# Kernel optimization log

Hardware: AMD Instinct MI355X
Metric: run time of the kernel (lower is better)

## Reference

```python
import jax, jax.numpy as jnp
import numpy as np

D = 1024
H = 16
DK = D // H
FF = int(8 / 3 * D)  # 2730
EPS = 1e-6


def setup_inputs() -> dict:
    key = jax.random.key(0)
    ks = jax.random.split(key, 8)
    s = lambda n: 1.0 / np.sqrt(n)
    return {
        "x": jax.random.normal(ks[0], (2, 2048, D), dtype=jnp.float32),
        "w_qkv": jax.random.normal(ks[1], (3 * D, D), dtype=jnp.float32) * s(D),
        "w_o": jax.random.normal(ks[2], (D, D), dtype=jnp.float32) * s(D),
        "n1_w": jnp.ones((D,), dtype=jnp.float32),
        "n2_w": jnp.ones((D,), dtype=jnp.float32),
        "w1": jax.random.normal(ks[3], (FF, D), dtype=jnp.float32) * s(D),
        "w2": jax.random.normal(ks[4], (D, FF), dtype=jnp.float32) * s(FF),
        "w3": jax.random.normal(ks[5], (FF, D), dtype=jnp.float32) * s(D),
    }


def _rmsnorm(x, w):
    return x * jax.lax.rsqrt(jnp.mean(x * x, axis=-1, keepdims=True) + EPS) * w


def _attn(x, w_qkv, w_o):
    B, L, _ = x.shape
    qkv = x @ w_qkv.T                       # [B,L,3D]
    qkv = qkv.reshape(B, L, 3, H, DK)
    q, k, v = qkv[:, :, 0], qkv[:, :, 1], qkv[:, :, 2]   # [B,L,H,DK]
    scores = jnp.einsum("blhd,bmhd->bhlm", q, k) / np.sqrt(DK).astype(np.float32)
    attn = jax.nn.softmax(scores, axis=-1)               # [B,H,L,L]
    out = jnp.einsum("bhlm,bmhd->blhd", attn, v).reshape(B, L, D)
    return out @ w_o.T


def _swiglu(x, w1, w2, w3):
    return (jax.nn.silu(x @ w1.T) * (x @ w3.T)) @ w2.T


def reference(x, w_qkv, w_o, n1_w, n2_w, w1, w2, w3):
    x = x + _attn(_rmsnorm(x, n1_w), w_qkv, w_o)
    return x + _swiglu(_rmsnorm(x, n2_w), w1, w2, w3)
```

## Files before the change

kernel.cpp:

```cpp
#include <hip/hip_runtime.h>
#include <stdint.h>


#define LSEQ   2048
#define DMODEL 1024
#define NHEAD  16
#define NTOK   4096
#define FFR    2730
#define FFP    2816
#define FF2    5632

typedef short  short8  __attribute__((ext_vector_type(8)));
typedef float  floatx4 __attribute__((ext_vector_type(4)));

__device__ __forceinline__ uint16_t f2bf(float f) {
  uint32_t u = __builtin_bit_cast(uint32_t, f);
  u += 0x7FFFu + ((u >> 16) & 1u);
  return (uint16_t)(u >> 16);
}
__device__ __forceinline__ float bf2f(uint16_t s) {
  uint32_t u = ((uint32_t)s) << 16;
  return __builtin_bit_cast(float, u);
}
__device__ __forceinline__ void gl2lds16(const void* g, void* l) {
  __builtin_amdgcn_global_load_lds(
      (const __attribute__((address_space(1))) unsigned int*)g,
      (__attribute__((address_space(3))) unsigned int*)l, 16, 0, 0);
}

__global__ __launch_bounds__(256) void cvt_all_k(const float* __restrict__ wqkv,
                                                 const float* __restrict__ wo,
                                                 const float* __restrict__ w1,
                                                 const float* __restrict__ w3,
                                                 uint16_t* __restrict__ dst) {
  int g = blockIdx.x;
  int c = threadIdx.x * 4;
  const float* src = nullptr;
  if (g < 3072)       src = wqkv + (size_t)g * 1024;
  else if (g < 4096)  src = wo + (size_t)(g - 3072) * 1024;
  else {
    int r = g - 4096;
    int u = r >> 6, wi = r & 63;
    int srow = u * 32 + (wi & 31);
    if (srow < FFR) src = ((wi < 32) ? w1 : w3) + (size_t)srow * 1024;
  }
  float4 v = src ? *(const float4*)(src + c) : float4{0, 0, 0, 0};
  uint64_t pack =  (uint64_t)f2bf(v.x)        | ((uint64_t)f2bf(v.y) << 16)
                | ((uint64_t)f2bf(v.z) << 32) | ((uint64_t)f2bf(v.w) << 48);
  *(uint64_t*)(dst + (size_t)g * 1024 + c) = pack;
}

__global__ void cvt_pad_k(const float* __restrict__ src, uint16_t* __restrict__ dst,
                          int rows, int cols, int cols_p, long total) {
  long idx = (long)blockIdx.x * 256 + threadIdx.x;
  if (idx >= total) return;
  int r = (int)(idx / cols_p);
  int c = (int)(idx % cols_p);
  float v = (r < rows && c < cols) ? src[(size_t)r * cols + c] : 0.0f;
  dst[idx] = f2bf(v);
}

__global__ __launch_bounds__(256) void rmsnorm_k(const float* __restrict__ x,
                                                 const float* __restrict__ wgt,
                                                 uint16_t* __restrict__ out) {
  const int row = blockIdx.x;
  const int c = threadIdx.x * 4;
  const float* xr = x + (size_t)row * DMODEL;
  float4 v = *(const float4*)(xr + c);
  float ss = v.x * v.x + v.y * v.y + v.z * v.z + v.w * v.w;
#pragma unroll
  for (int off = 32; off >= 1; off >>= 1) ss += __shfl_down(ss, off, 64);
  __shared__ float red[4];
  if ((threadIdx.x & 63) == 0) red[threadIdx.x >> 6] = ss;
  __syncthreads();
  float tot = red[0] + red[1] + red[2] + red[3];
  float scale = rsqrtf(tot * (1.0f / DMODEL) + 1e-6f);
  float4 wv = *(const float4*)(wgt + c);
  uint64_t pack =  (uint64_t)f2bf(v.x * scale * wv.x)
                | ((uint64_t)f2bf(v.y * scale * wv.y) << 16)
                | ((uint64_t)f2bf(v.z * scale * wv.z) << 32)
                | ((uint64_t)f2bf(v.w * scale * wv.w) << 48);
  *(uint64_t*)(out + (size_t)row * DMODEL + c) = pack;
}

template <int MODE, int TM, int TN>
__global__ __launch_bounds__(256) void gemm_bt(const uint16_t* __restrict__ A,
                                               const uint16_t* __restrict__ B,
                                               uint16_t* __restrict__ Cb,
                                               float* __restrict__ Cf,
                                               const float* __restrict__ Res,
                                               int M, int N, int K) {
  constexpr int FI = TM / 32, FJ = TN / 32;
  constexpr int NIT = (TM + TN) / 64;
  __shared__ uint16_t As[TM * 32];
  __shared__ uint16_t Bs[TN * 32];
  const int tid = threadIdx.x;
  const int w = tid >> 6, lane = tid & 63;
  const int grp = lane >> 4, l16 = lane & 15;
  const int m0 = blockIdx.y * TM, n0 = blockIdx.x * TN;
  const int rw = (w >> 1) * (TM / 2), cw = (w & 1) * (TN / 2);

  floatx4 acc[FI][FJ] = {};

  const uint16_t* gp[NIT];
  uint16_t* lp[NIT];
#pragma unroll
  for (int i = 0; i < NIT; i++) {
    int c = i * 256 + tid;
    if (c < TM * 4) {
      gp[i] = A + (size_t)(m0 + (c >> 2)) * K + (c & 3) * 8;
      lp[i] = As + c * 8;
    } else {
      int c2 = c - TM * 4;
      gp[i] = B + (size_t)(n0 + (c2 >> 2)) * K + (c2 & 3) * 8;
      lp[i] = Bs + c2 * 8;
    }
  }

  for (int k0 = 0; k0 < K; k0 += 32) {
#pragma unroll
    for (int i = 0; i < NIT; i++) gl2lds16(gp[i] + k0, lp[i]);
    __syncthreads();
    short8 af[FI], bfr[FJ];
#pragma unroll
    for (int i = 0; i < FI; i++)
      af[i] = *(const short8*)(As + (rw + i * 16 + l16) * 32 + grp * 8);
#pragma unroll
    for (int j = 0; j < FJ; j++)
      bfr[j] = *(const short8*)(Bs + (cw + j * 16 + l16) * 32 + grp * 8);
#pragma unroll
    for (int i = 0; i < FI; i++)
#pragma unroll
      for (int j = 0; j < FJ; j++)
        acc[i][j] = __builtin_amdgcn_mfma_f32_16x16x32_bf16(af[i], bfr[j], acc[i][j], 0, 0, 0);
    __syncthreads();
  }

  if constexpr (MODE == 2) {
    const int half = N >> 1;
#pragma unroll
    for (int i = 0; i < FI; i++) {
      const int mrow = m0 + rw + i * 16 + grp * 4;
#pragma unroll
      for (int j = 0; j < 2; j++) {
        const int gcol = (n0 >> 1) + (cw >> 1) + j * 16 + l16;
#pragma unroll
        for (int r = 0; r < 4; r++) {
          float a = acc[i][j][r];
          float bv = acc[i][j + 2][r];
          float ex = __builtin_amdgcn_exp2f(-a * 1.4426950408889634f);
          float s = a * __builtin_amdgcn_rcpf(1.0f + ex);
          Cb[(size_t)(mrow + r) * half + gcol] = f2bf(s * bv);
        }
      }
    }
  } else {
#pragma unroll
    for (int i = 0; i < FI; i++) {
#pragma unroll
      for (int j = 0; j < FJ; j++) {
        const int mrow = m0 + rw + i * 16 + grp * 4;
        const int ncol = n0 + cw + j * 16 + l16;
#pragma unroll
        for (int r = 0; r < 4; r++) {
          size_t idx = (size_t)(mrow + r) * N + ncol;
          float v = acc[i][j][r];
          if (MODE == 0) Cb[idx] = f2bf(v);
          else           Cf[idx] = v + Res[idx];
        }
      }
    }
  }
}

__global__ __launch_bounds__(256) void attn_flash(const uint16_t* __restrict__ qkv,
                                                  uint16_t* __restrict__ outp) {
  const int tid = threadIdx.x;
  const int w = tid >> 6, lane = tid & 63;
  const int grp = lane >> 4, l16 = lane & 15;
  const int lin = blockIdx.x;
  const int xcd = lin & 7;
  const int slot = lin >> 3;
  const int pair = xcd * 4 + (slot >> 4);
  const int qc = slot & 15;
  const int h = pair & 15, b = pair >> 4;
  const int q0 = qc * 128;

  __shared__ uint16_t Qs[8192];
  __shared__ uint16_t Ks[2][4096];
  __shared__ uint16_t Vt[2][64 * 76];
  __shared__ uint16_t Ps[128 * 76];

  const size_t base = ((size_t)b * LSEQ) * 3072 + (size_t)h * 64;

#pragma unroll
  for (int i = 0; i < 4; i++) {
    int c = i * 256 + tid;
    int row = c >> 3, cc = (c & 7) ^ (row & 7);
    gl2lds16(qkv + base + (size_t)(q0 + row) * 3072 + cc * 8, Qs + c * 8);
  }
#pragma unroll
  for (int i = 0; i < 2; i++) {
    int c = i * 256 + tid;
    int row = c >> 3, cc = (c & 7) ^ (row & 7);
    gl2lds16(qkv + base + (size_t)row * 3072 + 1024 + cc * 8, Ks[0] + c * 8);
  }
#pragma unroll
  for (int i = 0; i < 2; i++) {
    int c = i * 256 + tid;
    int tt = c & 63, db = c >> 6;
    uint4 vv = *(const uint4*)(qkv + base + (size_t)tt * 3072 + 2048 + db * 8);
    uint32_t uu[4] = {vv.x, vv.y, vv.z, vv.w};
#pragma unroll
    for (int e = 0; e < 4; e++) {
      Vt[0][(db * 8 + e * 2 + 0) * 76 + tt] = (uint16_t)(uu[e] & 0xFFFFu);
      Vt[0][(db * 8 + e * 2 + 1) * 76 + tt] = (uint16_t)(uu[e] >> 16);
    }
  }
  __syncthreads();

  short8 aq[2][2];
#pragma unroll
  for (int fi = 0; fi < 2; fi++) {
    const int qrow = w * 32 + fi * 16 + l16;
#pragma unroll
    for (int kk = 0; kk < 2; kk++) {
      int cc = kk * 4 + grp;
      aq[fi][kk] = *(const short8*)(Qs + (qrow * 8 + (cc ^ (qrow & 7))) * 8);
    }
  }

  float lsum[2][4] = {};
  floatx4 o_acc[2][4] = {};
  const float C = 0.125f * 1.4426950408889634f;

  for (int kc = 0; kc < LSEQ / 64; kc++) {
    const int cur = kc & 1, nxt = cur ^ 1;
    const bool pre = (kc + 1 < LSEQ / 64);
    const int t1 = (kc + 1) * 64;
    uint4 vv[2];
    if (pre) {
#pragma unroll
      for (int i = 0; i < 2; i++) {
        int c = i * 256 + tid;
        int row = c >> 3, cc = (c & 7) ^ (row & 7);
        gl2lds16(qkv + base + (size_t)(t1 + row) * 3072 + 1024 + cc * 8, Ks[nxt] + c * 8);
      }
#pragma unroll
      for (int i = 0; i < 2; i++) {
        int c = i * 256 + tid;
        int tt = c & 63, db = c >> 6;
        vv[i] = *(const uint4*)(qkv + base + (size_t)(t1 + tt) * 3072 + 2048 + db * 8);
      }
    }

    floatx4 s_acc[2][4] = {};
#pragma unroll
    for (int j = 0; j < 4; j++) {
      const int krow = j * 16 + l16;
#pragma unroll
      for (int kk = 0; kk < 2; kk++) {
        int cc = kk * 4 + grp;
        short8 bk = *(const short8*)(Ks[cur] + (krow * 8 + (cc ^ (krow & 7))) * 8);
#pragma unroll
        for (int fi = 0; fi < 2; fi++)
          s_acc[fi][j] = __builtin_amdgcn_mfma_f32_16x16x32_bf16(aq[fi][kk], bk, s_acc[fi][j], 0, 0, 0);
      }
    }

#pragma unroll
    for (int fi = 0; fi < 2; fi++) {
      const int prow = w * 32 + fi * 16 + grp * 4;
#pragma unroll
      for (int j = 0; j < 4; j++)
#pragma unroll
        for (int r = 0; r < 4; r++) {
          float pv = __builtin_amdgcn_exp2f(s_acc[fi][j][r] * C);
          lsum[fi][r] += pv;
          Ps[(prow + r) * 76 + j * 16 + l16] = f2bf(pv);
        }
    }

#pragma unroll
    for (int kk = 0; kk < 2; kk++) {
      short8 ap0 = *(const short8*)(Ps + (w * 32 + l16) * 76 + kk * 32 + grp * 8);
      short8 ap1 = *(const short8*)(Ps + (w * 32 + 16 + l16) * 76 + kk * 32 + grp * 8);
#pragma unroll
      for (int jj = 0; jj < 4; jj++) {
        short8 bv = *(const short8*)(Vt[cur] + (jj * 16 + l16) * 76 + kk * 32 + grp * 8);
        o_acc[0][jj] = __builtin_amdgcn_mfma_f32_16x16x32_bf16(ap0, bv, o_acc[0][jj], 0, 0, 0);
        o_acc[1][jj] = __builtin_amdgcn_mfma_f32_16x16x32_bf16(ap1, bv, o_acc[1][jj], 0, 0, 0);
      }
    }

    if (pre) {
#pragma unroll
      for (int i = 0; i < 2; i++) {
        int c = i * 256 + tid;
        int tt = c & 63, db = c >> 6;
        uint32_t uu[4] = {vv[i].x, vv[i].y, vv[i].z, vv[i].w};
#pragma unroll
        for (int e = 0; e < 4; e++) {
          Vt[nxt][(db * 8 + e * 2 + 0) * 76 + tt] = (uint16_t)(uu[e] & 0xFFFFu);
          Vt[nxt][(db * 8 + e * 2 + 1) * 76 + tt] = (uint16_t)(uu[e] >> 16);
        }
      }
    }
    __syncthreads();
  }

#pragma unroll
  for (int off = 8; off >= 1; off >>= 1)
#pragma unroll
    for (int fi = 0; fi < 2; fi++)
#pragma unroll
      for (int r = 0; r < 4; r++) lsum[fi][r] += __shfl_xor(lsum[fi][r], off, 64);
#pragma unroll
  for (int fi = 0; fi < 2; fi++)
#pragma unroll
    for (int jj = 0; jj < 4; jj++)
#pragma unroll
      for (int r = 0; r < 4; r++) {
        int row = b * LSEQ + q0 + w * 32 + fi * 16 + grp * 4 + r;
        float o = o_acc[fi][jj][r] * __builtin_amdgcn_rcpf(lsum[fi][r]);
        outp[(size_t)row * DMODEL + h * 64 + jj * 16 + l16] = f2bf(o);
      }
}

extern "C" void kernel_launch(void* const* d_in, const int* in_sizes, int n_in,
                              void* d_out, int out_size, void* d_ws, size_t ws_size,
                              hipStream_t stream) {
  const float* x    = (const float*)d_in[0];
  const float* wqkv = (const float*)d_in[1];
  const float* wo   = (const float*)d_in[2];
  const float* n1w  = (const float*)d_in[3];
  const float* n2w  = (const float*)d_in[4];
  const float* w1   = (const float*)d_in[5];
  const float* w2   = (const float*)d_in[6];
  const float* w3   = (const float*)d_in[7];
  float* out = (float*)d_out;

  char* p = (char*)d_ws;
  uint16_t* wall  = (uint16_t*)p; p += (size_t)9728 * 1024 * 2;
  uint16_t* wqkvb = wall;
  uint16_t* wob   = wall + (size_t)3072 * 1024;
  uint16_t* w13b  = wall + (size_t)4096 * 1024;
  uint16_t* w2b   = (uint16_t*)p; p += (size_t)1024 * FFP * 2;
  uint16_t* h1    = (uint16_t*)p; p += (size_t)NTOK * DMODEL * 2;
  uint16_t* qkvb  = (uint16_t*)p; p += (size_t)NTOK * 3072 * 2;
  uint16_t* attno = (uint16_t*)p; p += (size_t)NTOK * DMODEL * 2;
  float*    x1    = (float*)p;    p += (size_t)NTOK * DMODEL * 4;
  uint16_t* h2    = (uint16_t*)p; p += (size_t)NTOK * DMODEL * 2;
  uint16_t* gbuf  = (uint16_t*)p; p += (size_t)NTOK * FFP * 2;

  cvt_all_k<<<9728, 256, 0, stream>>>(wqkv, wo, w1, w3, wall);
  cvt_pad_k<<<(1024 * FFP) / 256, 256, 0, stream>>>(w2, w2b, 1024, FFR, FFP, 1024L * FFP);

  rmsnorm_k<<<NTOK, 256, 0, stream>>>(x, n1w, h1);
  gemm_bt<0, 128, 128><<<dim3(3072 / 128, NTOK / 128), 256, 0, stream>>>(
      h1, wqkvb, qkvb, nullptr, nullptr, NTOK, 3072, 1024);
  attn_flash<<<512, 256, 0, stream>>>(qkvb, attno);
  gemm_bt<1, 128, 64><<<dim3(1024 / 64, NTOK / 128), 256, 0, stream>>>(
      attno, wob, nullptr, x1, x, NTOK, 1024, 1024);
  rmsnorm_k<<<NTOK, 256, 0, stream>>>(x1, n2w, h2);
  gemm_bt<2, 128, 128><<<dim3(FF2 / 128, NTOK / 128), 256, 0, stream>>>(
      h2, w13b, gbuf, nullptr, nullptr, NTOK, FF2, 1024);
  gemm_bt<1, 128, 64><<<dim3(1024 / 64, NTOK / 128), 256, 0, stream>>>(
      gbuf, w2b, nullptr, out, x1, NTOK, 1024, FFP);
}
```

Baseline: 389.6 us.

## Halve attention query tile to 64 rows and load Q directly into registers

The flash-attention kernel now processes 64 query rows per block instead of 128, with one 16-row fragment per wave, and launches 1024 blocks instead of 512. Q fragments are read straight from global memory into registers, so the Q LDS buffer is gone and the P buffer shrinks. A launch-bounds occupancy hint of 3 is added. The goal is more blocks and waves per CU and lower register and LDS pressure, at the cost of loading each K/V chunk twice as often and doing fewer MFMAs per LDS read.

```diff
diff --git a/kernel.cpp b/kernel.cpp
--- a/kernel.cpp
+++ b/kernel.cpp
@@ -17,10 +17,6 @@
   uint32_t u = __builtin_bit_cast(uint32_t, f);
   u += 0x7FFFu + ((u >> 16) & 1u);
   return (uint16_t)(u >> 16);
-}
-__device__ __forceinline__ float bf2f(uint16_t s) {
-  uint32_t u = ((uint32_t)s) << 16;
-  return __builtin_bit_cast(float, u);
 }
 __device__ __forceinline__ void gl2lds16(const void* g, void* l) {
   __builtin_amdgcn_global_load_lds(
@@ -173,32 +169,32 @@
   }
 }
 
-__global__ __launch_bounds__(256) void attn_flash(const uint16_t* __restrict__ qkv,
-                                                  uint16_t* __restrict__ outp) {
+__global__ __launch_bounds__(256, 3) void attn_flash(const uint16_t* __restrict__ qkv,
+                                                     uint16_t* __restrict__ outp) {
   const int tid = threadIdx.x;
   const int w = tid >> 6, lane = tid & 63;
   const int grp = lane >> 4, l16 = lane & 15;
   const int lin = blockIdx.x;
   const int xcd = lin & 7;
   const int slot = lin >> 3;
-  const int pair = xcd * 4 + (slot >> 4);
-  const int qc = slot & 15;
+  const int pair = xcd * 4 + (slot >> 5);
+  const int qc = slot & 31;
   const int h = pair & 15, b = pair >> 4;
-  const int q0 = qc * 128;
-
-  __shared__ uint16_t Qs[8192];
+  const int q0 = qc * 64;
+
   __shared__ uint16_t Ks[2][4096];
   __shared__ uint16_t Vt[2][64 * 76];
-  __shared__ uint16_t Ps[128 * 76];
+  __shared__ uint16_t Ps[64 * 76];
 
   const size_t base = ((size_t)b * LSEQ) * 3072 + (size_t)h * 64;
 
-#pragma unroll
-  for (int i = 0; i < 4; i++) {
-    int c = i * 256 + tid;
-    int row = c >> 3, cc = (c & 7) ^ (row & 7);
-    gl2lds16(qkv + base + (size_t)(q0 + row) * 3072 + cc * 8, Qs + c * 8);
-  }
+  short8 aq[2];
+  {
+    const uint16_t* qr = qkv + base + (size_t)(q0 + w * 16 + l16) * 3072;
+    aq[0] = *(const short8*)(qr + grp * 8);
+    aq[1] = *(const short8*)(qr + 32 + grp * 8);
+  }
+
 #pragma unroll
   for (int i = 0; i < 2; i++) {
     int c = i * 256 + tid;
@@ -219,19 +215,8 @@
   }
   __syncthreads();
 
-  short8 aq[2][2];
-#pragma unroll
-  for (int fi = 0; fi < 2; fi++) {
-    const int qrow = w * 32 + fi * 16 + l16;
-#pragma unroll
-    for (int kk = 0; kk < 2; kk++) {
-      int cc = kk * 4 + grp;
-      aq[fi][kk] = *(const short8*)(Qs + (qrow * 8 + (cc ^ (qrow & 7))) * 8);
-    }
-  }
-
-  float lsum[2][4] = {};
-  floatx4 o_acc[2][4] = {};
+  float lsum[4] = {};
+  floatx4 o_acc[4] = {};
   const float C = 0.125f * 1.4426950408889634f;
 
   for (int kc = 0; kc < LSEQ / 64; kc++) {
@@ -254,7 +239,7 @@
       }
     }
 
-    floatx4 s_acc[2][4] = {};
+    floatx4 s_acc[4] = {};
 #pragma unroll
     for (int j = 0; j < 4; j++) {
       const int krow = j * 16 + l16;
@@ -262,34 +247,28 @@
       for (int kk = 0; kk < 2; kk++) {
         int cc = kk * 4 + grp;
         short8 bk = *(const short8*)(Ks[cur] + (krow * 8 + (cc ^ (krow & 7))) * 8);
-#pragma unroll
-        for (int fi = 0; fi < 2; fi++)
-          s_acc[fi][j] = __builtin_amdgcn_mfma_f32_16x16x32_bf16(aq[fi][kk], bk, s_acc[fi][j], 0, 0, 0);
-      }
-    }
-
-#pragma unroll
-    for (int fi = 0; fi < 2; fi++) {
-      const int prow = w * 32 + fi * 16 + grp * 4;
-#pragma unroll
-      for (int j = 0; j < 4; j++)
-#pragma unroll
-        for (int r = 0; r < 4; r++) {
-          float pv = __builtin_amdgcn_exp2f(s_acc[fi][j][r] * C);
-          lsum[fi][r] += pv;
-          Ps[(prow + r) * 76 + j * 16 + l16] = f2bf(pv);
-        }
+        s_acc[j] = __builtin_amdgcn_mfma_f32_16x16x32_bf16(aq[kk], bk, s_acc[j], 0, 0, 0);
+      }
+    }
+
+#pragma unroll
+    for (int j = 0; j < 4; j++) {
+      const int prow = w * 16 + grp * 4;
+#pragma unroll
+      for (int r = 0; r < 4; r++) {
+        float pv = __builtin_amdgcn_exp2f(s_acc[j][r] * C);
+        lsum[r] += pv;
+        Ps[(prow + r) * 76 + j * 16 + l16] = f2bf(pv);
+      }
     }
 
 #pragma unroll
     for (int kk = 0; kk < 2; kk++) {
-      short8 ap0 = *(const short8*)(Ps + (w * 32 + l16) * 76 + kk * 32 + grp * 8);
-      short8 ap1 = *(const short8*)(Ps + (w * 32 + 16 + l16) * 76 + kk * 32 + grp * 8);
+      short8 ap = *(const short8*)(Ps + (w * 16 + l16) * 76 + kk * 32 + grp * 8);
 #pragma unroll
       for (int jj = 0; jj < 4; jj++) {
         short8 bv = *(const short8*)(Vt[cur] + (jj * 16 + l16) * 76 + kk * 32 + grp * 8);
-        o_acc[0][jj] = __builtin_amdgcn_mfma_f32_16x16x32_bf16(ap0, bv, o_acc[0][jj], 0, 0, 0);
-        o_acc[1][jj] = __builtin_amdgcn_mfma_f32_16x16x32_bf16(ap1, bv, o_acc[1][jj], 0, 0, 0);
+        o_acc[jj] = __builtin_amdgcn_mfma_f32_16x16x32_bf16(ap, bv, o_acc[jj], 0, 0, 0);
       }
     }
 
@@ -312,19 +291,15 @@
 #pragma unroll
   for (int off = 8; off >= 1; off >>= 1)
 #pragma unroll
-    for (int fi = 0; fi < 2; fi++)
-#pragma unroll
-      for (int r = 0; r < 4; r++) lsum[fi][r] += __shfl_xor(lsum[fi][r], off, 64);
-#pragma unroll
-  for (int fi = 0; fi < 2; fi++)
-#pragma unroll
-    for (int jj = 0; jj < 4; jj++)
-#pragma unroll
-      for (int r = 0; r < 4; r++) {
-        int row = b * LSEQ + q0 + w * 32 + fi * 16 + grp * 4 + r;
-        float o = o_acc[fi][jj][r] * __builtin_amdgcn_rcpf(lsum[fi][r]);
-        outp[(size_t)row * DMODEL + h * 64 + jj * 16 + l16] = f2bf(o);
-      }
+    for (int r = 0; r < 4; r++) lsum[r] += __shfl_xor(lsum[r], off, 64);
+#pragma unroll
+  for (int jj = 0; jj < 4; jj++)
+#pragma unroll
+    for (int r = 0; r < 4; r++) {
+      int row = b * LSEQ + q0 + w * 16 + grp * 4 + r;
+      float o = o_acc[jj][r] * __builtin_amdgcn_rcpf(lsum[r]);
+      outp[(size_t)row * DMODEL + h * 64 + jj * 16 + l16] = f2bf(o);
+    }
 }
 
 extern "C" void kernel_launch(void* const* d_in, const int* in_sizes, int n_in,
@@ -359,7 +334,7 @@
   rmsnorm_k<<<NTOK, 256, 0, stream>>>(x, n1w, h1);
   gemm_bt<0, 128, 128><<<dim3(3072 / 128, NTOK / 128), 256, 0, stream>>>(
       h1, wqkvb, qkvb, nullptr, nullptr, NTOK, 3072, 1024);
-  attn_flash<<<512, 256, 0, stream>>>(qkvb, attno);
+  attn_flash<<<1024, 256, 0, stream>>>(qkvb, attno);
   gemm_bt<1, 128, 64><<<dim3(1024 / 64, NTOK / 128), 256, 0, stream>>>(
       attno, wob, nullptr, x1, x, NTOK, 1024, 1024);
   rmsnorm_k<<<NTOK, 256, 0, stream>>>(x1, n2w, h2);
```

Result: slower. 409.7 us (+5.2%).

## Transpose QK^T MFMA operands for packed P stores and drop Q LDS staging

Applied to the files above, without the earlier changes.

The attention kernel now loads Q straight from global memory into registers instead of staging it through LDS. It swaps the operands of the QK^T MFMA so each lane holds consecutive key scores for one query row. This lets P be written to LDS as packed 8-byte stores using v_cvt_pk_bf16, and the row-sum reduction becomes one value per lane with cross-group shuffles. The change also shrinks the LDS padding stride from 76 to 72 and asks for two blocks per CU, which lowers LDS use and per-thread register budget but may change bank conflicts or cause spills.

```diff
diff --git a/kernel.cpp b/kernel.cpp
--- a/kernel.cpp
+++ b/kernel.cpp
@@ -18,9 +18,10 @@
   u += 0x7FFFu + ((u >> 16) & 1u);
   return (uint16_t)(u >> 16);
 }
-__device__ __forceinline__ float bf2f(uint16_t s) {
-  uint32_t u = ((uint32_t)s) << 16;
-  return __builtin_bit_cast(float, u);
+__device__ __forceinline__ uint32_t cvt_pk_bf16(float a, float b) {
+  uint32_t d;
+  asm("v_cvt_pk_bf16_f32 %0, %1, %2" : "=v"(d) : "v"(a), "v"(b));
+  return d;
 }
 __device__ __forceinline__ void gl2lds16(const void* g, void* l) {
   __builtin_amdgcn_global_load_lds(
@@ -173,8 +174,8 @@
   }
 }
 
-__global__ __launch_bounds__(256) void attn_flash(const uint16_t* __restrict__ qkv,
-                                                  uint16_t* __restrict__ outp) {
+__global__ __launch_bounds__(256, 2) void attn_flash(const uint16_t* __restrict__ qkv,
+                                                     uint16_t* __restrict__ outp) {
   const int tid = threadIdx.x;
   const int w = tid >> 6, lane = tid & 63;
   const int grp = lane >> 4, l16 = lane & 15;
@@ -186,19 +187,20 @@
   const int h = pair & 15, b = pair >> 4;
   const int q0 = qc * 128;
 
-  __shared__ uint16_t Qs[8192];
   __shared__ uint16_t Ks[2][4096];
-  __shared__ uint16_t Vt[2][64 * 76];
-  __shared__ uint16_t Ps[128 * 76];
+  __shared__ uint16_t Vt[2][64 * 72];
+  __shared__ uint16_t Ps[128 * 72];
 
   const size_t base = ((size_t)b * LSEQ) * 3072 + (size_t)h * 64;
 
-#pragma unroll
-  for (int i = 0; i < 4; i++) {
-    int c = i * 256 + tid;
-    int row = c >> 3, cc = (c & 7) ^ (row & 7);
-    gl2lds16(qkv + base + (size_t)(q0 + row) * 3072 + cc * 8, Qs + c * 8);
-  }
+  short8 aq[2][2];
+#pragma unroll
+  for (int fi = 0; fi < 2; fi++) {
+    const uint16_t* qr = qkv + base + (size_t)(q0 + w * 32 + fi * 16 + l16) * 3072;
+    aq[fi][0] = *(const short8*)(qr + grp * 8);
+    aq[fi][1] = *(const short8*)(qr + 32 + grp * 8);
+  }
+
 #pragma unroll
   for (int i = 0; i < 2; i++) {
     int c = i * 256 + tid;
@@ -213,24 +215,13 @@
     uint32_t uu[4] = {vv.x, vv.y, vv.z, vv.w};
 #pragma unroll
     for (int e = 0; e < 4; e++) {
-      Vt[0][(db * 8 + e * 2 + 0) * 76 + tt] = (uint16_t)(uu[e] & 0xFFFFu);
-      Vt[0][(db * 8 + e * 2 + 1) * 76 + tt] = (uint16_t)(uu[e] >> 16);
+      Vt[0][(db * 8 + e * 2 + 0) * 72 + tt] = (uint16_t)(uu[e] & 0xFFFFu);
+      Vt[0][(db * 8 + e * 2 + 1) * 72 + tt] = (uint16_t)(uu[e] >> 16);
     }
   }
   __syncthreads();
 
-  short8 aq[2][2];
-#pragma unroll
-  for (int fi = 0; fi < 2; fi++) {
-    const int qrow = w * 32 + fi * 16 + l16;
-#pragma unroll
-    for (int kk = 0; kk < 2; kk++) {
-      int cc = kk * 4 + grp;
-      aq[fi][kk] = *(const short8*)(Qs + (qrow * 8 + (cc ^ (qrow & 7))) * 8);
-    }
-  }
-
-  float lsum[2][4] = {};
+  float lsum[2] = {};
   floatx4 o_acc[2][4] = {};
   const float C = 0.125f * 1.4426950408889634f;
 
@@ -254,7 +245,7 @@
       }
     }
 
-    floatx4 s_acc[2][4] = {};
+    floatx4 s_acc[4][2] = {};
 #pragma unroll
     for (int j = 0; j < 4; j++) {
       const int krow = j * 16 + l16;
@@ -264,30 +255,32 @@
         short8 bk = *(const short8*)(Ks[cur] + (krow * 8 + (cc ^ (krow & 7))) * 8);
 #pragma unroll
         for (int fi = 0; fi < 2; fi++)
-          s_acc[fi][j] = __builtin_amdgcn_mfma_f32_16x16x32_bf16(aq[fi][kk], bk, s_acc[fi][j], 0, 0, 0);
-      }
-    }
-
-#pragma unroll
-    for (int fi = 0; fi < 2; fi++) {
-      const int prow = w * 32 + fi * 16 + grp * 4;
-#pragma unroll
-      for (int j = 0; j < 4; j++)
-#pragma unroll
-        for (int r = 0; r < 4; r++) {
-          float pv = __builtin_amdgcn_exp2f(s_acc[fi][j][r] * C);
-          lsum[fi][r] += pv;
-          Ps[(prow + r) * 76 + j * 16 + l16] = f2bf(pv);
-        }
-    }
+          s_acc[j][fi] = __builtin_amdgcn_mfma_f32_16x16x32_bf16(bk, aq[fi][kk], s_acc[j][fi], 0, 0, 0);
+      }
+    }
+
+#pragma unroll
+    for (int j = 0; j < 4; j++)
+#pragma unroll
+      for (int fi = 0; fi < 2; fi++) {
+        float p0 = __builtin_amdgcn_exp2f(s_acc[j][fi][0] * C);
+        float p1 = __builtin_amdgcn_exp2f(s_acc[j][fi][1] * C);
+        float p2 = __builtin_amdgcn_exp2f(s_acc[j][fi][2] * C);
+        float p3 = __builtin_amdgcn_exp2f(s_acc[j][fi][3] * C);
+        lsum[fi] += (p0 + p1) + (p2 + p3);
+        uint2 pk;
+        pk.x = cvt_pk_bf16(p0, p1);
+        pk.y = cvt_pk_bf16(p2, p3);
+        *(uint2*)(Ps + (w * 32 + fi * 16 + l16) * 72 + j * 16 + grp * 4) = pk;
+      }
 
 #pragma unroll
     for (int kk = 0; kk < 2; kk++) {
-      short8 ap0 = *(const short8*)(Ps + (w * 32 + l16) * 76 + kk * 32 + grp * 8);
-      short8 ap1 = *(const short8*)(Ps + (w * 32 + 16 + l16) * 76 + kk * 32 + grp * 8);
+      short8 ap0 = *(const short8*)(Ps + (w * 32 + l16) * 72 + kk * 32 + grp * 8);
+      short8 ap1 = *(const short8*)(Ps + (w * 32 + 16 + l16) * 72 + kk * 32 + grp * 8);
 #pragma unroll
       for (int jj = 0; jj < 4; jj++) {
-        short8 bv = *(const short8*)(Vt[cur] + (jj * 16 + l16) * 76 + kk * 32 + grp * 8);
+        short8 bv = *(const short8*)(Vt[cur] + (jj * 16 + l16) * 72 + kk * 32 + grp * 8);
         o_acc[0][jj] = __builtin_amdgcn_mfma_f32_16x16x32_bf16(ap0, bv, o_acc[0][jj], 0, 0, 0);
         o_acc[1][jj] = __builtin_amdgcn_mfma_f32_16x16x32_bf16(ap1, bv, o_acc[1][jj], 0, 0, 0);
       }
@@ -301,8 +294,8 @@
         uint32_t uu[4] = {vv[i].x, vv[i].y, vv[i].z, vv[i].w};
 #pragma unroll
         for (int e = 0; e < 4; e++) {
-          Vt[nxt][(db * 8 + e * 2 + 0) * 76 + tt] = (uint16_t)(uu[e] & 0xFFFFu);
-          Vt[nxt][(db * 8 + e * 2 + 1) * 76 + tt] = (uint16_t)(uu[e] >> 16);
+          Vt[nxt][(db * 8 + e * 2 + 0) * 72 + tt] = (uint16_t)(uu[e] & 0xFFFFu);
+          Vt[nxt][(db * 8 + e * 2 + 1) * 72 + tt] = (uint16_t)(uu[e] >> 16);
         }
       }
     }
@@ -310,11 +303,16 @@
   }
 
 #pragma unroll
-  for (int off = 8; off >= 1; off >>= 1)
-#pragma unroll
-    for (int fi = 0; fi < 2; fi++)
-#pragma unroll
-      for (int r = 0; r < 4; r++) lsum[fi][r] += __shfl_xor(lsum[fi][r], off, 64);
+  for (int fi = 0; fi < 2; fi++) {
+    lsum[fi] += __shfl_xor(lsum[fi], 16, 64);
+    lsum[fi] += __shfl_xor(lsum[fi], 32, 64);
+  }
+  float lsr[2][4];
+#pragma unroll
+  for (int fi = 0; fi < 2; fi++)
+#pragma unroll
+    for (int r = 0; r < 4; r++)
+      lsr[fi][r] = __shfl(lsum[fi], grp * 4 + r, 64);
 #pragma unroll
   for (int fi = 0; fi < 2; fi++)
 #pragma unroll
@@ -322,7 +320,7 @@
 #pragma unroll
       for (int r = 0; r < 4; r++) {
         int row = b * LSEQ + q0 + w * 32 + fi * 16 + grp * 4 + r;
-        float o = o_acc[fi][jj][r] * __builtin_amdgcn_rcpf(lsum[fi][r]);
+        float o = o_acc[fi][jj][r] * __builtin_amdgcn_rcpf(lsr[fi][r]);
         outp[(size_t)row * DMODEL + h * 64 + jj * 16 + l16] = f2bf(o);
       }
 }
```

Result: faster. 368.4 us (-5.4%).
